# Performance work log

Hardware: AMD Instinct MI355X
Metric: run time of the kernel (lower is better)

Reference implementation:

```python
import jax, jax.numpy as jnp
import numpy as np

EMBED_DIM = 4096
POLY_PTS = 32
POLY_DIM = POLY_PTS * 2  # 64
LN_EPS = 1e-5


def setup_inputs() -> dict:
    key = jax.random.key(0)
    ks = jax.random.split(key, 12)
    B, N, Dmax = 8, 1024, POLY_DIM
    s = 0.02
    return {
        "prompts": jax.random.normal(ks[0], (B, N, Dmax), dtype=jnp.float32),
        "prompt_types": jax.random.randint(ks[1], (B, N), 0, 3, dtype=jnp.int64),
        # point encoder: Linear(2, E)
        "point_w": jax.random.normal(ks[2], (EMBED_DIM, 2), dtype=jnp.float32) * s,
        "point_b": jax.random.normal(ks[3], (EMBED_DIM,), dtype=jnp.float32) * s,
        # box encoder: Linear(4, E)
        "box_w": jax.random.normal(ks[4], (EMBED_DIM, 4), dtype=jnp.float32) * s,
        "box_b": jax.random.normal(ks[5], (EMBED_DIM,), dtype=jnp.float32) * s,
        # polygon encoder: Linear(64,E) -> LayerNorm(E) -> ReLU -> Linear(E,E)
        "poly_w1": jax.random.normal(ks[6], (EMBED_DIM, POLY_DIM), dtype=jnp.float32) * s,
        "poly_b1": jax.random.normal(ks[7], (EMBED_DIM,), dtype=jnp.float32) * s,
        "ln_gamma": jnp.ones((EMBED_DIM,), dtype=jnp.float32),
        "ln_beta": jnp.zeros((EMBED_DIM,), dtype=jnp.float32),
        "poly_w2": jax.random.normal(ks[8], (EMBED_DIM, EMBED_DIM), dtype=jnp.float32) * s,
        "poly_b2": jax.random.normal(ks[9], (EMBED_DIM,), dtype=jnp.float32) * s,
        # type embedding table (3, E)
        "type_emb": jax.random.normal(ks[10], (3, EMBED_DIM), dtype=jnp.float32) * s,
    }


def _layernorm(x, gamma, beta):
    mu = jnp.mean(x, axis=-1, keepdims=True)
    var = jnp.mean(jnp.square(x - mu), axis=-1, keepdims=True)
    return (x - mu) * jax.lax.rsqrt(var + LN_EPS) * gamma + beta


def reference(prompts, prompt_types, point_w, point_b, box_w, box_b,
              poly_w1, poly_b1, ln_gamma, ln_beta, poly_w2, poly_b2, type_emb):
    # Per-type expert encodings computed densely, then selected by type mask
    # (same math as torch's masked gather -> linear -> scatter).
    pt = jnp.einsum('bnd,ed->bne', prompts[..., :2], point_w) + point_b + type_emb[0]
    bx = jnp.einsum('bnd,ed->bne', prompts[..., :4], box_w) + box_b + type_emb[1]
    h = jnp.einsum('bnd,ed->bne', prompts[..., :POLY_DIM], poly_w1) + poly_b1
    h = jax.nn.relu(_layernorm(h, ln_gamma, ln_beta))
    pg = jnp.einsum('bnd,ed->bne', h, poly_w2) + poly_b2 + type_emb[2]
    t = prompt_types[..., None]
    zeros = jnp.zeros_like(pt)
    out = jnp.where(t == 0, pt, zeros) + jnp.where(t == 1, bx, zeros) + jnp.where(t == 2, pg, zeros)
    return out
```

## Files before the change

kernel.cpp:

```cpp
#include <hip/hip_runtime.h>

#define EMBED 4096
#define NTOK 8192
#define LN_EPS 1e-5f

#define NB_CONVW2 (EMBED * EMBED / (256 * 8))
#define NB_CONVW1 (EMBED * 64 / (256 * 8))

typedef float f4_t __attribute__((ext_vector_type(4)));
typedef __bf16 bf16x8 __attribute__((ext_vector_type(8)));
typedef unsigned short us8_t __attribute__((ext_vector_type(8)));

__device__ __forceinline__ unsigned short f2bf(float f) {
    unsigned int u = __float_as_uint(f);
    u += 0x7fffu + ((u >> 16) & 1u);
    return (unsigned short)(u >> 16);
}

typedef const __attribute__((address_space(1))) unsigned int gas_t;
typedef __attribute__((address_space(3))) unsigned int las_t;

__device__ __forceinline__ void gl_lds16(const void* g, void* l) {
    __builtin_amdgcn_global_load_lds((gas_t*)g, (las_t*)l, 16, 0, 0);
}

__device__ __forceinline__ void conv_body(const float* __restrict__ src,
                                          unsigned short* __restrict__ dst,
                                          int i) {
    const f4_t* in4 = (const f4_t*)src;
    f4_t v0 = in4[(size_t)i * 2];
    f4_t v1 = in4[(size_t)i * 2 + 1];
    us8_t o;
    o[0] = f2bf(v0.x); o[1] = f2bf(v0.y); o[2] = f2bf(v0.z); o[3] = f2bf(v0.w);
    o[4] = f2bf(v1.x); o[5] = f2bf(v1.y); o[6] = f2bf(v1.z); o[7] = f2bf(v1.w);
    *(us8_t*)(dst + (size_t)i * 8) = o;
}

__global__ __launch_bounds__(256) void k_prep(
    const float* __restrict__ prompts, const int* __restrict__ types,
    const float* __restrict__ pw, const float* __restrict__ pb,
    const float* __restrict__ bw, const float* __restrict__ bb,
    const float* __restrict__ temb,
    const float* __restrict__ w1, const float* __restrict__ b1,
    const float* __restrict__ w2,
    int* __restrict__ idx, int* __restrict__ counters,
    float* __restrict__ G, float* __restrict__ cbar,
    unsigned short* __restrict__ w1b, unsigned short* __restrict__ w2b,
    float* __restrict__ out)
{
    int bid = blockIdx.x;
    int t = threadIdx.x;

    if (bid == 0) {
        __shared__ int cnt;
        if (t == 0) cnt = 0;
        __syncthreads();
        for (int i = t; i < NTOK; i += 256) {
            if (types[i] == 2) {
                int s = atomicAdd(&cnt, 1);
                idx[s] = i;
            }
        }
        __syncthreads();
        if (t == 0) {
            counters[0] = cnt;
            counters[1] = (cnt + 127) & ~127;
        }
        return;
    }

    if (bid <= 66) {
        int i = bid - 1;
        __shared__ float sA[64][66];
        int wave = t >> 6, lane = t & 63;
        float part[17];
#pragma unroll
        for (int jj = 0; jj < 17; ++jj) part[jj] = 0.f;
        for (int e0 = 0; e0 < EMBED; e0 += 64) {
            __syncthreads();
#pragma unroll
            for (int q = 0; q < 4; ++q) {
                int v = t + 256 * q;
                int r = v >> 4, c4 = v & 15;
                f4_t val = *(const f4_t*)(w1 + (size_t)(e0 + r) * 64 + c4 * 4);
                sA[r][c4 * 4 + 0] = val.x;
                sA[r][c4 * 4 + 1] = val.y;
                sA[r][c4 * 4 + 2] = val.z;
                sA[r][c4 * 4 + 3] = val.w;
            }
            if (t < 64) sA[t][64] = b1[e0 + t];
            __syncthreads();
            float ai = (i < 65) ? sA[lane][i] : 1.f;
#pragma unroll
            for (int jj = 0; jj < 16; ++jj)
                part[jj] += ai * sA[lane][wave * 16 + jj];
            if (wave == 3) part[16] += ai * sA[lane][64];
        }
#pragma unroll
        for (int jj = 0; jj < 17; ++jj) {
            float v = part[jj];
            v += __shfl_down(v, 32);
            v += __shfl_down(v, 16);
            v += __shfl_down(v, 8);
            v += __shfl_down(v, 4);
            v += __shfl_down(v, 2);
            v += __shfl_down(v, 1);
            part[jj] = v;
        }
        if (lane == 0) {
            int nj = (wave == 3) ? 17 : 16;
            for (int jj = 0; jj < nj; ++jj) {
                int j = (jj == 16) ? 64 : (wave * 16 + jj);
                float s = part[jj] * (1.f / 4096.f);
                if (i < 65) G[i * 65 + j] = s;
                else        cbar[j] = s;
            }
        }
        return;
    }

    if (bid < 67 + NB_CONVW2) {
        conv_body(w2, w2b, (bid - 67) * 256 + t);
        return;
    }

    if (bid < 67 + NB_CONVW2 + NB_CONVW1) {
        conv_body(w1, w1b, (bid - 67 - NB_CONVW2) * 256 + t);
        return;
    }

    {
        int token = bid - (67 + NB_CONVW2 + NB_CONVW1);
        int ty = types[token];
        if (ty >= 2) return;
        const float* x = prompts + (size_t)token * 64;
        float x0 = x[0], x1 = x[1], x2 = x[2], x3 = x[3];
        f4_t* o4 = (f4_t*)(out + (size_t)token * EMBED);
        if (ty == 0) {
            const f4_t* w4 = (const f4_t*)pw;
            const f4_t* b4 = (const f4_t*)pb;
            const f4_t* te4 = (const f4_t*)temb;
#pragma unroll
            for (int j = 0; j < 4; ++j) {
                int e4 = t + 256 * j;
                f4_t wa = w4[e4 * 2], wb = w4[e4 * 2 + 1];
                f4_t bv = b4[e4], tv = te4[e4];
                f4_t r;
                r.x = x0 * wa.x + x1 * wa.y + bv.x + tv.x;
                r.y = x0 * wa.z + x1 * wa.w + bv.y + tv.y;
                r.z = x0 * wb.x + x1 * wb.y + bv.z + tv.z;
                r.w = x0 * wb.z + x1 * wb.w + bv.w + tv.w;
                o4[e4] = r;
            }
        } else {
            const f4_t* w4 = (const f4_t*)bw;
            const f4_t* b4 = (const f4_t*)bb;
            const f4_t* te4 = (const f4_t*)(temb + EMBED);
#pragma unroll
            for (int j = 0; j < 4; ++j) {
                int e4 = t + 256 * j;
                f4_t w0 = w4[e4 * 4 + 0], w1v = w4[e4 * 4 + 1];
                f4_t w2v = w4[e4 * 4 + 2], w3v = w4[e4 * 4 + 3];
                f4_t bv = b4[e4], tv = te4[e4];
                f4_t r;
                r.x = x0 * w0.x + x1 * w0.y + x2 * w0.z + x3 * w0.w + bv.x + tv.x;
                r.y = x0 * w1v.x + x1 * w1v.y + x2 * w1v.z + x3 * w1v.w + bv.y + tv.y;
                r.z = x0 * w2v.x + x1 * w2v.y + x2 * w2v.z + x3 * w2v.w + bv.z + tv.z;
                r.w = x0 * w3v.x + x1 * w3v.y + x2 * w3v.z + x3 * w3v.w + bv.w + tv.w;
                o4[e4] = r;
            }
        }
    }
}

__global__ __launch_bounds__(256) void k_stats(const float* __restrict__ prompts,
                                               const int* __restrict__ idx,
                                               const int* __restrict__ counters,
                                               const float* __restrict__ cbar,
                                               const float* __restrict__ G,
                                               float* __restrict__ mu,
                                               float* __restrict__ rstd,
                                               unsigned short* __restrict__ xbuf) {
    int count = counters[0], padded = counters[1];
    int base = blockIdx.x * 4;
    if (base >= padded) return;
    __shared__ float sG[65 * 65];
    __shared__ __align__(16) float xs[4][66];
    int t = threadIdx.x;
    for (int v = t; v < 65 * 65; v += 256) sG[v] = G[v];
    int r = t >> 6, lane = t & 63;
    int m = base + r;
    bool vld = (m < count);
    float xv = vld ? prompts[(size_t)idx[m] * 64 + lane] : 0.f;
    xs[r][lane] = xv;
    if (lane == 0) xs[r][64] = vld ? 1.f : 0.f;
    xbuf[(size_t)m * 64 + lane] = vld ? f2bf(xv) : (unsigned short)0;
    __syncthreads();
    float mu_p, m2_p;
    {
        float xi = xs[r][lane];
        mu_p = cbar[lane] * xi;
        const float* Gr = sG + lane * 65;
        float rd = 0.f;
        for (int j = 0; j < 65; ++j) rd += Gr[j] * xs[r][j];
        m2_p = xi * rd;
    }
    if (lane == 0) {
        float xi = xs[r][64];
        mu_p += cbar[64] * xi;
        const float* Gr = sG + 64 * 65;
        float rd = 0.f;
        for (int j = 0; j < 65; ++j) rd += Gr[j] * xs[r][j];
        m2_p += xi * rd;
    }
    for (int off = 32; off > 0; off >>= 1) {
        mu_p += __shfl_down(mu_p, off);
        m2_p += __shfl_down(m2_p, off);
    }
    if (lane == 0) {
        if (vld) {
            mu[m] = mu_p;
            rstd[m] = rsqrtf(fmaxf(m2_p - mu_p * mu_p, 0.f) + LN_EPS);
        } else {
            mu[m] = 0.f;
            rstd[m] = 0.f;
        }
    }
}

__global__ __launch_bounds__(256) void k_lin1m(const unsigned short* __restrict__ xbuf,
                                               const unsigned short* __restrict__ w1b,
                                               const int* __restrict__ counters,
                                               const float* __restrict__ b1,
                                               const float* __restrict__ gamma,
                                               const float* __restrict__ beta,
                                               const float* __restrict__ mu,
                                               const float* __restrict__ rstd,
                                               unsigned short* __restrict__ hbuf) {
    int padded = counters[1];
    int m0 = blockIdx.y * 128;
    if (m0 >= padded) return;
    int n0 = blockIdx.x * 128;

    __shared__ unsigned short At[128 * 32];
    __shared__ unsigned short Bt[128 * 32];

    int t = threadIdx.x;
    int lane = t & 63, wave = t >> 6;
    int wm = (wave >> 1) * 64;
    int wn = (wave & 1) * 64;

    int srow = t >> 2, skg = t & 3;
    const unsigned short* Ag = xbuf + (size_t)(m0 + srow) * 64 + skg * 8;
    const unsigned short* Bg = w1b + (size_t)(n0 + srow) * 64 + skg * 8;
    char* AtC = (char*)At;
    char* BtC = (char*)Bt;
    int ldsw = (t & ~63) * 16;

    f4_t acc[4][4];
#pragma unroll
    for (int i = 0; i < 4; ++i)
#pragma unroll
        for (int j = 0; j < 4; ++j) acc[i][j] = (f4_t)0.f;

    int fr = lane & 15;
    int quad = lane >> 4;

#pragma unroll
    for (int k0 = 0; k0 < 64; k0 += 32) {
        __syncthreads();
        gl_lds16(Ag + k0,            AtC + ldsw);
        gl_lds16(Ag + 64 * 64 + k0,  AtC + 4096 + ldsw);
        gl_lds16(Bg + k0,            BtC + ldsw);
        gl_lds16(Bg + 64 * 64 + k0,  BtC + 4096 + ldsw);
        __syncthreads();

        bf16x8 a[4], b[4];
#pragma unroll
        for (int i = 0; i < 4; ++i) {
            a[i] = *(const bf16x8*)(AtC + (wm + i * 16 + fr) * 64 + quad * 16);
            b[i] = *(const bf16x8*)(BtC + (wn + i * 16 + fr) * 64 + quad * 16);
        }
#pragma unroll
        for (int i = 0; i < 4; ++i)
#pragma unroll
            for (int j = 0; j < 4; ++j)
                acc[i][j] = __builtin_amdgcn_mfma_f32_16x16x32_bf16(a[i], b[j], acc[i][j], 0, 0, 0);
    }

#pragma unroll
    for (int i = 0; i < 4; ++i) {
#pragma unroll
        for (int r = 0; r < 4; ++r) {
            int grow = m0 + wm + i * 16 + quad * 4 + r;
            float muv = mu[grow], rsv = rstd[grow];
            unsigned short* hrow = hbuf + (size_t)grow * EMBED;
#pragma unroll
            for (int j = 0; j < 4; ++j) {
                int gcol = n0 + wn + j * 16 + fr;
                float h = (acc[i][j][r] + b1[gcol] - muv) * rsv * gamma[gcol] + beta[gcol];
                hrow[gcol] = f2bf(fmaxf(h, 0.f));
            }
        }
    }
}

__global__ __launch_bounds__(256) void k_gemm(const unsigned short* __restrict__ hbuf,
                                              const unsigned short* __restrict__ w2b,
                                              const int* __restrict__ idx,
                                              const int* __restrict__ counters,
                                              const float* __restrict__ b2,
                                              const float* __restrict__ te2,
                                              float* __restrict__ out) {
    int count = counters[0], padded = counters[1];
    int m0 = blockIdx.y * 128;
    if (m0 >= padded) return;
    int n0 = blockIdx.x * 128;

    __shared__ unsigned short At[128 * 32];
    __shared__ unsigned short Bt[128 * 32];

    int t = threadIdx.x;
    int lane = t & 63, wave = t >> 6;
    int wm = (wave >> 1) * 64;
    int wn = (wave & 1) * 64;

    int srow = t >> 2, skg = t & 3;
    const unsigned short* Ag = hbuf + (size_t)(m0 + srow) * EMBED + skg * 8;
    const unsigned short* Bg = w2b + (size_t)(n0 + srow) * EMBED + skg * 8;
    char* AtC = (char*)At;
    char* BtC = (char*)Bt;
    int ldsw = (t & ~63) * 16;

    f4_t acc[4][4];
#pragma unroll
    for (int i = 0; i < 4; ++i)
#pragma unroll
        for (int j = 0; j < 4; ++j) acc[i][j] = (f4_t)0.f;

    int fr = lane & 15;
    int quad = lane >> 4;

    for (int k0 = 0; k0 < EMBED; k0 += 32) {
        __syncthreads();
        gl_lds16(Ag + k0,               AtC + ldsw);
        gl_lds16(Ag + 64 * EMBED + k0,  AtC + 4096 + ldsw);
        gl_lds16(Bg + k0,               BtC + ldsw);
        gl_lds16(Bg + 64 * EMBED + k0,  BtC + 4096 + ldsw);
        __syncthreads();

        bf16x8 a[4], b[4];
#pragma unroll
        for (int i = 0; i < 4; ++i) {
            a[i] = *(const bf16x8*)(AtC + (wm + i * 16 + fr) * 64 + quad * 16);
            b[i] = *(const bf16x8*)(BtC + (wn + i * 16 + fr) * 64 + quad * 16);
        }
#pragma unroll
        for (int i = 0; i < 4; ++i)
#pragma unroll
            for (int j = 0; j < 4; ++j)
                acc[i][j] = __builtin_amdgcn_mfma_f32_16x16x32_bf16(a[i], b[j], acc[i][j], 0, 0, 0);
    }

#pragma unroll
    for (int i = 0; i < 4; ++i) {
#pragma unroll
        for (int r = 0; r < 4; ++r) {
            int grow = m0 + wm + i * 16 + quad * 4 + r;
            if (grow < count) {
                float* orow = out + (size_t)idx[grow] * EMBED;
#pragma unroll
                for (int j = 0; j < 4; ++j) {
                    int gcol = n0 + wn + j * 16 + fr;
                    orow[gcol] = acc[i][j][r] + b2[gcol] + te2[gcol];
                }
            }
        }
    }
}

extern "C" void kernel_launch(void* const* d_in, const int* in_sizes, int n_in,
                              void* d_out, int out_size, void* d_ws, size_t ws_size,
                              hipStream_t stream) {
    const float* prompts  = (const float*)d_in[0];
    const int*   types    = (const int*)d_in[1];
    const float* point_w  = (const float*)d_in[2];
    const float* point_b  = (const float*)d_in[3];
    const float* box_w    = (const float*)d_in[4];
    const float* box_b    = (const float*)d_in[5];
    const float* poly_w1  = (const float*)d_in[6];
    const float* poly_b1  = (const float*)d_in[7];
    const float* ln_g     = (const float*)d_in[8];
    const float* ln_b     = (const float*)d_in[9];
    const float* poly_w2  = (const float*)d_in[10];
    const float* poly_b2  = (const float*)d_in[11];
    const float* type_emb = (const float*)d_in[12];
    float* out = (float*)d_out;

    char* ws = (char*)d_ws;
    int*   counters = (int*)ws;
    int*   idx      = (int*)(ws + 256);
    float* cbar     = (float*)(ws + 33280);
    float* G        = (float*)(ws + 33792);
    float* muarr    = (float*)(ws + 51200);
    float* rstdarr  = (float*)(ws + 84224);
    unsigned short* xbuf = (unsigned short*)(ws + 131072);
    unsigned short* w1b  = (unsigned short*)(ws + 131072 + 1048576);
    unsigned short* w2b  = (unsigned short*)(ws + 2097152);
    unsigned short* hbuf = (unsigned short*)(ws + 2097152 + (size_t)EMBED * EMBED * 2);

    int nprep = 67 + NB_CONVW2 + NB_CONVW1 + NTOK;
    k_prep<<<nprep, 256, 0, stream>>>(prompts, types, point_w, point_b,
                                      box_w, box_b, type_emb,
                                      poly_w1, poly_b1, poly_w2,
                                      idx, counters, G, cbar, w1b, w2b, out);
    k_stats<<<NTOK / 4, 256, 0, stream>>>(prompts, idx, counters, cbar, G,
                                          muarr, rstdarr, xbuf);
    k_lin1m<<<dim3(EMBED / 128, NTOK / 128), 256, 0, stream>>>(
        xbuf, w1b, counters, poly_b1, ln_g, ln_b, muarr, rstdarr, hbuf);
    k_gemm<<<dim3(EMBED / 128, NTOK / 128), 256, 0, stream>>>(
        hbuf, w2b, idx, counters, poly_b2, type_emb + 2 * EMBED, out);
}
```

Measured before the change: 382.5 us.

## Rewrite second GEMM with 256x256 tiles, double-buffered swizzled LDS pipeline

The second polygon GEMM moves from 128x128 tiles with 256 threads and a single-buffered K=32 loop to 256x256 tiles with 512 threads. It adds two 64-wide K stages in 128KB of dynamic LDS, an XOR-swizzled layout, and prefetches of the next stage interleaved with MFMA phases under explicit waitcnt, barrier and setprio control. Row padding is raised to 256 to match the tile. The goal is to hide global-load latency and raise data reuse per LDS byte. The cost is fewer blocks than CUs, which can leave the GPU underfilled, plus heavy register and LDS use.

```diff
diff --git a/kernel.cpp b/kernel.cpp
--- a/kernel.cpp
+++ b/kernel.cpp
@@ -64,7 +64,7 @@
         __syncthreads();
         if (t == 0) {
             counters[0] = cnt;
-            counters[1] = (cnt + 127) & ~127;
+            counters[1] = (cnt + 255) & ~255;
         }
         return;
     }
@@ -305,74 +305,118 @@
     }
 }
 
-__global__ __launch_bounds__(256) void k_gemm(const unsigned short* __restrict__ hbuf,
-                                              const unsigned short* __restrict__ w2b,
-                                              const int* __restrict__ idx,
-                                              const int* __restrict__ counters,
-                                              const float* __restrict__ b2,
-                                              const float* __restrict__ te2,
-                                              float* __restrict__ out) {
+__global__ __launch_bounds__(512, 2) void k_gemm(const unsigned short* __restrict__ hbuf,
+                                                 const unsigned short* __restrict__ w2b,
+                                                 const int* __restrict__ idx,
+                                                 const int* __restrict__ counters,
+                                                 const float* __restrict__ b2,
+                                                 const float* __restrict__ te2,
+                                                 float* __restrict__ out) {
+    extern __shared__ char lds[];
     int count = counters[0], padded = counters[1];
-    int m0 = blockIdx.y * 128;
+    int m0 = blockIdx.y * 256;
     if (m0 >= padded) return;
-    int n0 = blockIdx.x * 128;
-
-    __shared__ unsigned short At[128 * 32];
-    __shared__ unsigned short Bt[128 * 32];
+    int n0 = blockIdx.x * 256;
 
     int t = threadIdx.x;
     int lane = t & 63, wave = t >> 6;
-    int wm = (wave >> 1) * 64;
-    int wn = (wave & 1) * 64;
-
-    int srow = t >> 2, skg = t & 3;
-    const unsigned short* Ag = hbuf + (size_t)(m0 + srow) * EMBED + skg * 8;
-    const unsigned short* Bg = w2b + (size_t)(n0 + srow) * EMBED + skg * 8;
-    char* AtC = (char*)At;
-    char* BtC = (char*)Bt;
-    int ldsw = (t & ~63) * 16;
-
-    f4_t acc[4][4];
-#pragma unroll
-    for (int i = 0; i < 4; ++i)
+    int wm = (wave >> 2) * 128;
+    int wn = (wave & 3) * 64;
+    int fr = lane & 15, quad = lane >> 4;
+
+    int srow = t >> 3;
+    int scg = (t & 7) ^ (srow & 7);
+    const unsigned short* Ag = hbuf + (size_t)(m0 + srow) * EMBED + scg * 8;
+    const unsigned short* Bg = w2b + (size_t)(n0 + srow) * EMBED + scg * 8;
+    char* ldsw = lds + wave * 1024;
+
+#define STAGE_A(ns, c, nko) gl_lds16(Ag + (size_t)(c) * 64 * EMBED + (nko), ldsw + (ns) * 32768 + (c) * 8192)
+#define STAGE_B(ns, c, nko) gl_lds16(Bg + (size_t)(c) * 64 * EMBED + (nko), ldsw + 65536 + (ns) * 32768 + (c) * 8192)
+
+    int swzk0 = ((quad ^ (fr & 7)) << 4);
+    int swzk1 = (((4 + quad) ^ (fr & 7)) << 4);
+
+    f4_t acc[8][4];
+#pragma unroll
+    for (int i = 0; i < 8; ++i)
 #pragma unroll
         for (int j = 0; j < 4; ++j) acc[i][j] = (f4_t)0.f;
 
-    int fr = lane & 15;
-    int quad = lane >> 4;
-
-    for (int k0 = 0; k0 < EMBED; k0 += 32) {
-        __syncthreads();
-        gl_lds16(Ag + k0,               AtC + ldsw);
-        gl_lds16(Ag + 64 * EMBED + k0,  AtC + 4096 + ldsw);
-        gl_lds16(Bg + k0,               BtC + ldsw);
-        gl_lds16(Bg + 64 * EMBED + k0,  BtC + 4096 + ldsw);
-        __syncthreads();
-
-        bf16x8 a[4], b[4];
-#pragma unroll
-        for (int i = 0; i < 4; ++i) {
-            a[i] = *(const bf16x8*)(AtC + (wm + i * 16 + fr) * 64 + quad * 16);
-            b[i] = *(const bf16x8*)(BtC + (wn + i * 16 + fr) * 64 + quad * 16);
-        }
-#pragma unroll
-        for (int i = 0; i < 4; ++i)
-#pragma unroll
-            for (int j = 0; j < 4; ++j)
-                acc[i][j] = __builtin_amdgcn_mfma_f32_16x16x32_bf16(a[i], b[j], acc[i][j], 0, 0, 0);
-    }
-
-#pragma unroll
-    for (int i = 0; i < 4; ++i) {
+    STAGE_A(0, 0, 0); STAGE_A(0, 2, 0);
+    STAGE_B(0, 0, 0); STAGE_B(0, 1, 0);
+    STAGE_B(0, 2, 0); STAGE_B(0, 3, 0);
+    STAGE_A(0, 1, 0); STAGE_A(0, 3, 0);
+    asm volatile("s_waitcnt vmcnt(0)" ::: "memory");
+    __builtin_amdgcn_s_barrier();
+
+    int ra = (wm + fr) * 128;
+    int rb = (wn + fr) * 128;
+
+    for (int kt = 0; kt < 64; ++kt) {
+        int s = kt & 1, ns = s ^ 1;
+        int nko = (kt + 1) * 64;
+        bool hn = (kt < 63);
+        const char* LA = lds + s * 32768;
+        const char* LB = lds + 65536 + s * 32768;
+
+#pragma unroll
+        for (int p = 0; p < 4; ++p) {
+            const int mh = p >> 1, kk = p & 1;
+            const int swz = kk ? 0 : 1;
+            (void)swz;
+            bf16x8 a[4], b[4];
+#pragma unroll
+            for (int mi4 = 0; mi4 < 4; ++mi4)
+                a[mi4] = *(const bf16x8*)(LA + ra + mh * 8192 + mi4 * 2048 + (kk ? swzk1 : swzk0));
+#pragma unroll
+            for (int nj = 0; nj < 4; ++nj)
+                b[nj] = *(const bf16x8*)(LB + rb + nj * 2048 + (kk ? swzk1 : swzk0));
+
+            if (hn) {
+                if (p == 0) { STAGE_A(ns, 0, nko); STAGE_A(ns, 2, nko); }
+                if (p == 1) { STAGE_B(ns, 0, nko); STAGE_B(ns, 1, nko); }
+                if (p == 2) { STAGE_B(ns, 2, nko); STAGE_B(ns, 3, nko); }
+                if (p == 3) { STAGE_A(ns, 1, nko); STAGE_A(ns, 3, nko); }
+            }
+            if (p == 1) {
+                if (hn) asm volatile("s_waitcnt vmcnt(4)" ::: "memory");
+                else    asm volatile("s_waitcnt vmcnt(0)" ::: "memory");
+            }
+            if (p == 3) asm volatile("s_waitcnt vmcnt(2)" ::: "memory");
+            __builtin_amdgcn_s_barrier();
+            asm volatile("s_waitcnt lgkmcnt(0)" ::: "memory");
+            __builtin_amdgcn_sched_barrier(0);
+            __builtin_amdgcn_s_setprio(1);
+#pragma unroll
+            for (int mi4 = 0; mi4 < 4; ++mi4)
+#pragma unroll
+                for (int nj = 0; nj < 4; ++nj)
+                    acc[mh * 4 + mi4][nj] = __builtin_amdgcn_mfma_f32_16x16x32_bf16(
+                        a[mi4], b[nj], acc[mh * 4 + mi4][nj], 0, 0, 0);
+            __builtin_amdgcn_s_setprio(0);
+            __builtin_amdgcn_s_barrier();
+        }
+    }
+#undef STAGE_A
+#undef STAGE_B
+
+    float addv[4];
+#pragma unroll
+    for (int nj = 0; nj < 4; ++nj) {
+        int gcol = n0 + wn + nj * 16 + fr;
+        addv[nj] = b2[gcol] + te2[gcol];
+    }
+#pragma unroll
+    for (int mi = 0; mi < 8; ++mi) {
 #pragma unroll
         for (int r = 0; r < 4; ++r) {
-            int grow = m0 + wm + i * 16 + quad * 4 + r;
+            int grow = m0 + wm + mi * 16 + quad * 4 + r;
             if (grow < count) {
                 float* orow = out + (size_t)idx[grow] * EMBED;
 #pragma unroll
-                for (int j = 0; j < 4; ++j) {
-                    int gcol = n0 + wn + j * 16 + fr;
-                    orow[gcol] = acc[i][j][r] + b2[gcol] + te2[gcol];
+                for (int nj = 0; nj < 4; ++nj) {
+                    int gcol = n0 + wn + nj * 16 + fr;
+                    orow[gcol] = acc[mi][nj][r] + addv[nj];
                 }
             }
         }
@@ -409,6 +453,9 @@
     unsigned short* w2b  = (unsigned short*)(ws + 2097152);
     unsigned short* hbuf = (unsigned short*)(ws + 2097152 + (size_t)EMBED * EMBED * 2);
 
+    (void)hipFuncSetAttribute((const void*)k_gemm,
+                              hipFuncAttributeMaxDynamicSharedMemorySize, 131072);
+
     int nprep = 67 + NB_CONVW2 + NB_CONVW1 + NTOK;
     k_prep<<<nprep, 256, 0, stream>>>(prompts, types, point_w, point_b,
                                       box_w, box_b, type_emb,
@@ -418,6 +465,6 @@
                                           muarr, rstdarr, xbuf);
     k_lin1m<<<dim3(EMBED / 128, NTOK / 128), 256, 0, stream>>>(
         xbuf, w1b, counters, poly_b1, ln_g, ln_b, muarr, rstdarr, hbuf);
-    k_gemm<<<dim3(EMBED / 128, NTOK / 128), 256, 0, stream>>>(
+    k_gemm<<<dim3(EMBED / 256, NTOK / 256), 512, 131072, stream>>>(
         hbuf, w2b, idx, counters, poly_b2, type_emb + 2 * EMBED, out);
 }
```

New measurement: 388.2 us. Within noise of the previous version (+1.5%).

## Fuse W2 bf16 conversion into GEMM B-tile loads and remap blocks

Applied to the files above, without the earlier changes.

Drops the separate pass in k_prep that converts poly_w2 from fp32 to bf16 into a workspace buffer. Each k_gemm block now loads fp32 W2 directly, converts it to bf16 in registers and writes it to LDS, prefetching the next k-slice into registers. The grid is also remapped into a compact list of active tiles, interleaved in groups of eight so neighbouring blocks share W2 columns. This removes a 64 MB fp32 read plus 32 MB bf16 write, but every M-tile now rereads W2 in fp32 (twice the bytes of bf16) and repeats the conversion, which adds ALU work and global traffic inside the GEMM main loop.

```diff
diff --git a/kernel.cpp b/kernel.cpp
--- a/kernel.cpp
+++ b/kernel.cpp
@@ -4,7 +4,6 @@
 #define NTOK 8192
 #define LN_EPS 1e-5f
 
-#define NB_CONVW2 (EMBED * EMBED / (256 * 8))
 #define NB_CONVW1 (EMBED * 64 / (256 * 8))
 
 typedef float f4_t __attribute__((ext_vector_type(4)));
@@ -42,10 +41,9 @@
     const float* __restrict__ bw, const float* __restrict__ bb,
     const float* __restrict__ temb,
     const float* __restrict__ w1, const float* __restrict__ b1,
-    const float* __restrict__ w2,
     int* __restrict__ idx, int* __restrict__ counters,
     float* __restrict__ G, float* __restrict__ cbar,
-    unsigned short* __restrict__ w1b, unsigned short* __restrict__ w2b,
+    unsigned short* __restrict__ w1b,
     float* __restrict__ out)
 {
     int bid = blockIdx.x;
@@ -119,18 +117,13 @@
         return;
     }
 
-    if (bid < 67 + NB_CONVW2) {
-        conv_body(w2, w2b, (bid - 67) * 256 + t);
+    if (bid < 67 + NB_CONVW1) {
+        conv_body(w1, w1b, (bid - 67) * 256 + t);
         return;
     }
 
-    if (bid < 67 + NB_CONVW2 + NB_CONVW1) {
-        conv_body(w1, w1b, (bid - 67 - NB_CONVW2) * 256 + t);
-        return;
-    }
-
     {
-        int token = bid - (67 + NB_CONVW2 + NB_CONVW1);
+        int token = bid - (67 + NB_CONVW1);
         int ty = types[token];
         if (ty >= 2) return;
         const float* x = prompts + (size_t)token * 64;
@@ -306,16 +299,20 @@
 }
 
 __global__ __launch_bounds__(256) void k_gemm(const unsigned short* __restrict__ hbuf,
-                                              const unsigned short* __restrict__ w2b,
+                                              const float* __restrict__ w2,
                                               const int* __restrict__ idx,
                                               const int* __restrict__ counters,
                                               const float* __restrict__ b2,
                                               const float* __restrict__ te2,
                                               float* __restrict__ out) {
     int count = counters[0], padded = counters[1];
-    int m0 = blockIdx.y * 128;
-    if (m0 >= padded) return;
-    int n0 = blockIdx.x * 128;
+    int flat = blockIdx.y * 32 + blockIdx.x;
+    int active = (padded >> 7) * 32;
+    if (flat >= active) return;
+    int q = active >> 3;
+    int nid = (flat & 7) * q + (flat >> 3);
+    int m0 = (nid >> 5) * 128;
+    int n0 = (nid & 31) * 128;
 
     __shared__ unsigned short At[128 * 32];
     __shared__ unsigned short Bt[128 * 32];
@@ -327,10 +324,12 @@
 
     int srow = t >> 2, skg = t & 3;
     const unsigned short* Ag = hbuf + (size_t)(m0 + srow) * EMBED + skg * 8;
-    const unsigned short* Bg = w2b + (size_t)(n0 + srow) * EMBED + skg * 8;
+    const float* Bg0 = w2 + (size_t)(n0 + srow) * EMBED + skg * 8;
+    const float* Bg1 = Bg0 + (size_t)64 * EMBED;
     char* AtC = (char*)At;
-    char* BtC = (char*)Bt;
     int ldsw = (t & ~63) * 16;
+    unsigned short* Bw0 = Bt + t * 8;
+    unsigned short* Bw1 = Bt + 64 * 32 + t * 8;
 
     f4_t acc[4][4];
 #pragma unroll
@@ -341,15 +340,38 @@
     int fr = lane & 15;
     int quad = lane >> 4;
 
+    f4_t pb00 = *(const f4_t*)(Bg0);
+    f4_t pb01 = *(const f4_t*)(Bg0 + 4);
+    f4_t pb10 = *(const f4_t*)(Bg1);
+    f4_t pb11 = *(const f4_t*)(Bg1 + 4);
+
     for (int k0 = 0; k0 < EMBED; k0 += 32) {
         __syncthreads();
         gl_lds16(Ag + k0,               AtC + ldsw);
         gl_lds16(Ag + 64 * EMBED + k0,  AtC + 4096 + ldsw);
-        gl_lds16(Bg + k0,               BtC + ldsw);
-        gl_lds16(Bg + 64 * EMBED + k0,  BtC + 4096 + ldsw);
-        __syncthreads();
+        {
+            us8_t o0, o1;
+            o0[0] = f2bf(pb00.x); o0[1] = f2bf(pb00.y);
+            o0[2] = f2bf(pb00.z); o0[3] = f2bf(pb00.w);
+            o0[4] = f2bf(pb01.x); o0[5] = f2bf(pb01.y);
+            o0[6] = f2bf(pb01.z); o0[7] = f2bf(pb01.w);
+            o1[0] = f2bf(pb10.x); o1[1] = f2bf(pb10.y);
+            o1[2] = f2bf(pb10.z); o1[3] = f2bf(pb10.w);
+            o1[4] = f2bf(pb11.x); o1[5] = f2bf(pb11.y);
+            o1[6] = f2bf(pb11.z); o1[7] = f2bf(pb11.w);
+            *(us8_t*)Bw0 = o0;
+            *(us8_t*)Bw1 = o1;
+        }
+        __syncthreads();
+        if (k0 + 32 < EMBED) {
+            pb00 = *(const f4_t*)(Bg0 + k0 + 32);
+            pb01 = *(const f4_t*)(Bg0 + k0 + 36);
+            pb10 = *(const f4_t*)(Bg1 + k0 + 32);
+            pb11 = *(const f4_t*)(Bg1 + k0 + 36);
+        }
 
         bf16x8 a[4], b[4];
+        char* BtC = (char*)Bt;
 #pragma unroll
         for (int i = 0; i < 4; ++i) {
             a[i] = *(const bf16x8*)(AtC + (wm + i * 16 + fr) * 64 + quad * 16);
@@ -406,18 +428,17 @@
     float* rstdarr  = (float*)(ws + 84224);
     unsigned short* xbuf = (unsigned short*)(ws + 131072);
     unsigned short* w1b  = (unsigned short*)(ws + 131072 + 1048576);
-    unsigned short* w2b  = (unsigned short*)(ws + 2097152);
     unsigned short* hbuf = (unsigned short*)(ws + 2097152 + (size_t)EMBED * EMBED * 2);
 
-    int nprep = 67 + NB_CONVW2 + NB_CONVW1 + NTOK;
+    int nprep = 67 + NB_CONVW1 + NTOK;
     k_prep<<<nprep, 256, 0, stream>>>(prompts, types, point_w, point_b,
                                       box_w, box_b, type_emb,
-                                      poly_w1, poly_b1, poly_w2,
-                                      idx, counters, G, cbar, w1b, w2b, out);
+                                      poly_w1, poly_b1,
+                                      idx, counters, G, cbar, w1b, out);
     k_stats<<<NTOK / 4, 256, 0, stream>>>(prompts, idx, counters, cbar, G,
                                           muarr, rstdarr, xbuf);
     k_lin1m<<<dim3(EMBED / 128, NTOK / 128), 256, 0, stream>>>(
         xbuf, w1b, counters, poly_b1, ln_g, ln_b, muarr, rstdarr, hbuf);
     k_gemm<<<dim3(EMBED / 128, NTOK / 128), 256, 0, stream>>>(
-        hbuf, w2b, idx, counters, poly_b2, type_emb + 2 * EMBED, out);
-}
+        hbuf, poly_w2, idx, counters, poly_b2, type_emb + 2 * EMBED, out);
+}
```

After: 416.9 us. 1.09x slower.

## Triple-buffer LDS tiles in the polygon GEMM to overlap loads with MFMA

Applied to the files above, without the earlier changes.

Replaces the single-buffered load-sync-compute loop in the second polygon GEMM with a three-stage LDS ring. Global-to-LDS loads run two K-steps ahead, and manual vmcnt waits plus one barrier per iteration replace the two full syncthreads. The goal is to hide global memory latency behind MFMA work. The cost is three times the LDS per block, which may reduce occupancy, and the code now depends on exact hand-written vmcnt counts for correctness.

```diff
diff --git a/kernel.cpp b/kernel.cpp
--- a/kernel.cpp
+++ b/kernel.cpp
@@ -317,8 +317,8 @@
     if (m0 >= padded) return;
     int n0 = blockIdx.x * 128;
 
-    __shared__ unsigned short At[128 * 32];
-    __shared__ unsigned short Bt[128 * 32];
+    __shared__ unsigned short At[3][128 * 32];
+    __shared__ unsigned short Bt[3][128 * 32];
 
     int t = threadIdx.x;
     int lane = t & 63, wave = t >> 6;
@@ -328,8 +328,6 @@
     int srow = t >> 2, skg = t & 3;
     const unsigned short* Ag = hbuf + (size_t)(m0 + srow) * EMBED + skg * 8;
     const unsigned short* Bg = w2b + (size_t)(n0 + srow) * EMBED + skg * 8;
-    char* AtC = (char*)At;
-    char* BtC = (char*)Bt;
     int ldsw = (t & ~63) * 16;
 
     f4_t acc[4][4];
@@ -341,14 +339,24 @@
     int fr = lane & 15;
     int quad = lane >> 4;
 
-    for (int k0 = 0; k0 < EMBED; k0 += 32) {
-        __syncthreads();
-        gl_lds16(Ag + k0,               AtC + ldsw);
-        gl_lds16(Ag + 64 * EMBED + k0,  AtC + 4096 + ldsw);
-        gl_lds16(Bg + k0,               BtC + ldsw);
-        gl_lds16(Bg + 64 * EMBED + k0,  BtC + 4096 + ldsw);
-        __syncthreads();
-
+#define STAGE(s, k0) do {                                   \
+        gl_lds16(Ag + (k0),             (char*)At[s] + ldsw);        \
+        gl_lds16(Ag + 64 * EMBED + (k0), (char*)At[s] + 4096 + ldsw); \
+        gl_lds16(Bg + (k0),             (char*)Bt[s] + ldsw);        \
+        gl_lds16(Bg + 64 * EMBED + (k0), (char*)Bt[s] + 4096 + ldsw); \
+    } while (0)
+
+    STAGE(0, 0);
+    STAGE(1, 32);
+    asm volatile("s_waitcnt vmcnt(4)" ::: "memory");
+    __builtin_amdgcn_s_barrier();
+
+    int cur = 0, stg = 2;
+    for (int kt = 0; kt < 128; ++kt) {
+        if (kt + 2 < 128) STAGE(stg, (kt + 2) * 32);
+
+        const char* AtC = (const char*)At[cur];
+        const char* BtC = (const char*)Bt[cur];
         bf16x8 a[4], b[4];
 #pragma unroll
         for (int i = 0; i < 4; ++i) {
@@ -360,7 +368,15 @@
 #pragma unroll
             for (int j = 0; j < 4; ++j)
                 acc[i][j] = __builtin_amdgcn_mfma_f32_16x16x32_bf16(a[i], b[j], acc[i][j], 0, 0, 0);
-    }
+
+        if (kt < 126) asm volatile("s_waitcnt vmcnt(4)" ::: "memory");
+        else          asm volatile("s_waitcnt vmcnt(0)" ::: "memory");
+        __builtin_amdgcn_s_barrier();
+
+        cur = (cur == 2) ? 0 : cur + 1;
+        stg = (stg == 2) ? 0 : stg + 1;
+    }
+#undef STAGE
 
 #pragma unroll
     for (int i = 0; i < 4; ++i) {
```

After: 384.2 us. Within noise of the previous version (+0.5%).
